# Performance work log

Hardware: AMD Instinct MI355X
Metric: run time of the kernel (lower is better)

Reference implementation:

```python
import jax, jax.numpy as jnp
import numpy as np

B, S, D, H = 64, 64, 4096, 64  # NOTE: code requires S == H (see notes)
HD = D // H  # 64


def setup_inputs() -> dict:
    key = jax.random.key(0)
    ks = jax.random.split(key, 9)
    std = 0.02
    return {
        "x": jax.random.normal(ks[0], (B, S, D), dtype=jnp.float32),
        "Wq": jax.random.normal(ks[1], (D, D), dtype=jnp.float32) * std,
        "bq": jax.random.normal(ks[2], (D,), dtype=jnp.float32) * std,
        "Wk": jax.random.normal(ks[3], (D, D), dtype=jnp.float32) * std,
        "bk": jax.random.normal(ks[4], (D,), dtype=jnp.float32) * std,
        "Wv": jax.random.normal(ks[5], (D, D), dtype=jnp.float32) * std,
        "bv": jax.random.normal(ks[6], (D,), dtype=jnp.float32) * std,
        "Wp": jax.random.normal(ks[7], (D, D), dtype=jnp.float32) * std,
        "bp": jax.random.normal(ks[8], (D,), dtype=jnp.float32) * std,
    }


def reference(x, Wq, bq, Wk, bk, Wv, bv, Wp, bp):
    b, s, d = x.shape
    h, hd = H, d // H
    # q, k: [B,S,D] -> [B,S,H,hd] -> [B,H,S,hd]
    q = (x @ Wq.T + bq).reshape(b, s, h, hd).transpose(0, 2, 1, 3)
    k = (x @ Wk.T + bk).reshape(b, s, h, hd).transpose(0, 2, 1, 3)
    # v: faithfully replicates the original buggy view(B, H, S, hd).transpose(1,2)
    # -> shape [B, S, H, hd] (NOT head-major)
    v = (x @ Wv.T + bv).reshape(b, h, s, hd).transpose(0, 2, 1, 3)
    # attention WITHOUT 1/sqrt(hd) scaling (faithful to source)
    attn = jax.nn.softmax(jnp.einsum("bhqd,bhkd->bhqk", q, k), axis=-1)  # [B,H,S,S]
    # dropout layers are identity in eval mode
    # ShardedTensor: chunk v along last dim into 2 shards of hd/2
    v0, v1 = jnp.split(v, 2, axis=-1)  # each [B,S,H,hd/2]; broadcast needs S==H
    out0 = jnp.matmul(attn, v0)  # [B,H,S,hd/2]
    out1 = jnp.matmul(attn, v1)
    out = jnp.concatenate([out0, out1], axis=0)  # [2B,H,S,hd/2] (faithful cat on dim 0)
    out = out.transpose(0, 2, 1, 3).reshape(b, s, d)  # row-major regroup, same as torch view
    return out @ Wp.T + bp
```

## Files before the change

kernel.cpp:

```cpp
#include <hip/hip_runtime.h>
#include <stdint.h>

typedef __bf16   bf16x8  __attribute__((ext_vector_type(8)));
typedef float    f32x4   __attribute__((ext_vector_type(4)));
typedef uint16_t u16x8   __attribute__((ext_vector_type(8)));

using as1_cvp = const __attribute__((address_space(1))) void*;
using as3_vp  = __attribute__((address_space(3))) void*;

__device__ __forceinline__ uint16_t f2bf(float f) {
    uint32_t u = __float_as_uint(f);
    u += 0x7FFF + ((u >> 16) & 1);
    return (uint16_t)(u >> 16);
}

__device__ __forceinline__ void gload16(const void* g, void* l) {
    __builtin_amdgcn_global_load_lds((as1_cvp)g, (as3_vp)l, 16, 0, 0);
}

#define MFMA16(a, b, c) __builtin_amdgcn_mfma_f32_16x16x32_bf16((a), (b), (c), 0, 0, 0)

__global__ __launch_bounds__(256)
void cvt_bf16(const float* __restrict__ in, uint16_t* __restrict__ out, int n8)
{
    int i = blockIdx.x * 256 + threadIdx.x;
    if (i >= n8) return;
    const float4* p = reinterpret_cast<const float4*>(in) + (size_t)i * 2;
    float4 a = p[0], b = p[1];
    u16x8 o;
    o[0] = f2bf(a.x); o[1] = f2bf(a.y); o[2] = f2bf(a.z); o[3] = f2bf(a.w);
    o[4] = f2bf(b.x); o[5] = f2bf(b.y); o[6] = f2bf(b.z); o[7] = f2bf(b.w);
    reinterpret_cast<u16x8*>(out)[i] = o;
}

__global__ __launch_bounds__(256)
void cvt5(const float* __restrict__ s0, const float* __restrict__ s1,
          const float* __restrict__ s2, const float* __restrict__ s3,
          const float* __restrict__ s4,
          uint16_t* __restrict__ d0, uint16_t* __restrict__ d1,
          uint16_t* __restrict__ d2, uint16_t* __restrict__ d3,
          uint16_t* __restrict__ d4)
{
    const int r = blockIdx.x >> 13;
    const float*  src = (r == 0) ? s0 : (r == 1) ? s1 : (r == 2) ? s2
                       : (r == 3) ? s3 : s4;
    uint16_t*     dst = (r == 0) ? d0 : (r == 1) ? d1 : (r == 2) ? d2
                       : (r == 3) ? d3 : d4;
    const int i = (blockIdx.x & 8191) * 256 + threadIdx.x;
    const float4* p = reinterpret_cast<const float4*>(src) + (size_t)i * 2;
    float4 a = p[0], b = p[1];
    u16x8 o;
    o[0] = f2bf(a.x); o[1] = f2bf(a.y); o[2] = f2bf(a.z); o[3] = f2bf(a.w);
    o[4] = f2bf(b.x); o[5] = f2bf(b.y); o[6] = f2bf(b.z); o[7] = f2bf(b.w);
    reinterpret_cast<u16x8*>(dst)[i] = o;
}

template <int OUT_BF16>
__global__ __launch_bounds__(512, 2)
void gemm256(const uint16_t* __restrict__ A, const uint16_t* __restrict__ Bt,
             const float* __restrict__ bias, void* __restrict__ Cout,
             int M, int N, int K)
{
    __shared__ uint16_t lds[65536];
    const int NT = K >> 6;

    int bid = blockIdx.x;
    bid = (bid & 7) * 32 + (bid >> 3);
    const int bx = bid & 15, by = bid >> 4;
    const int rb = by * 256, cb = bx * 256;

    const int tid  = threadIdx.x;
    const int w    = tid >> 6;
    const int lane = tid & 63;
    const int g    = lane >> 4;
    const int l16  = lane & 15;
    const int wm   = w >> 2;
    const int wn   = w & 3;
    const int srow = lane >> 2;
    const int sblk = lane & 3;

    f32x4 acc[8][4] = {};

    auto stageA = [&](int buf, int kh, int kbase) {
#pragma unroll
        for (int i = 0; i < 2; ++i) {
            const int row = i * 128 + w * 16 + srow;
            const uint16_t* src = A + (size_t)(rb + row) * K + kbase
                                    + ((sblk ^ ((row >> 1) & 3)) << 3);
            gload16(src, &lds[(buf * 2 + kh) * 16384 + i * 4096 + w * 512]);
        }
    };
    auto stageB = [&](int buf, int kh, int kbase) {
#pragma unroll
        for (int i = 0; i < 2; ++i) {
            const int row = i * 128 + w * 16 + srow;
            const uint16_t* src = Bt + (size_t)(cb + row) * K + kbase
                                     + ((sblk ^ ((row >> 1) & 3)) << 3);
            gload16(src, &lds[(buf * 2 + kh) * 16384 + 8192 + i * 4096 + w * 512]);
        }
    };

    auto readA = [&](int base, int grp, bf16x8* dst) {
#pragma unroll
        for (int mi = 0; mi < 4; ++mi) {
            const int r = wm * 128 + grp * 64 + mi * 16 + l16;
            dst[mi] = *reinterpret_cast<const bf16x8*>(
                &lds[base + r * 32 + ((g ^ ((r >> 1) & 3)) << 3)]);
        }
    };
    auto readB = [&](int base, bf16x8* dst) {
#pragma unroll
        for (int n = 0; n < 4; ++n) {
            const int c = wn * 64 + n * 16 + l16;
            dst[n] = *reinterpret_cast<const bf16x8*>(
                &lds[base + 8192 + c * 32 + ((g ^ ((c >> 1) & 3)) << 3)]);
        }
    };

    auto mfma_grp = [&](int grp, const bf16x8* af, const bf16x8* bf) {
        __builtin_amdgcn_s_setprio(1);
#pragma unroll
        for (int mi = 0; mi < 4; ++mi)
#pragma unroll
            for (int n = 0; n < 4; ++n)
                acc[grp * 4 + mi][n] = MFMA16(af[mi], bf[n], acc[grp * 4 + mi][n]);
        __builtin_amdgcn_s_setprio(0);
    };

    stageA(0, 0, 0);  stageB(0, 0, 0);
    stageA(0, 1, 32); stageB(0, 1, 32);
    stageA(1, 0, 64); stageB(1, 0, 64);
    asm volatile("s_waitcnt vmcnt(4)" ::: "memory");
    __builtin_amdgcn_s_barrier();

    for (int t = 0; t < NT; ++t) {
        const int cur = t & 1, nxt = cur ^ 1;
        const int b0 = (cur * 2 + 0) * 16384;
        const int b1 = (cur * 2 + 1) * 16384;
        bf16x8 af[4], bf[4];

        readA(b0, 0, af); readB(b0, bf);
        if (t + 1 < NT) stageA(nxt, 1, (t + 1) * 64 + 32);
        __builtin_amdgcn_s_barrier();
        asm volatile("s_waitcnt lgkmcnt(0)" ::: "memory");
        __builtin_amdgcn_sched_barrier(0);
        mfma_grp(0, af, bf);
        __builtin_amdgcn_sched_barrier(0);
        __builtin_amdgcn_s_barrier();

        readA(b0, 1, af);
        if (t + 1 < NT) stageB(nxt, 1, (t + 1) * 64 + 32);
        __builtin_amdgcn_s_barrier();
        asm volatile("s_waitcnt lgkmcnt(0)" ::: "memory");
        __builtin_amdgcn_sched_barrier(0);
        mfma_grp(1, af, bf);
        __builtin_amdgcn_sched_barrier(0);
        __builtin_amdgcn_s_barrier();

        readA(b1, 0, af); readB(b1, bf);
        if (t + 2 < NT) stageA(cur, 0, (t + 2) * 64);
        __builtin_amdgcn_s_barrier();
        asm volatile("s_waitcnt lgkmcnt(0)" ::: "memory");
        __builtin_amdgcn_sched_barrier(0);
        mfma_grp(0, af, bf);
        __builtin_amdgcn_sched_barrier(0);
        __builtin_amdgcn_s_barrier();

        readA(b1, 1, af);
        if (t + 2 < NT) stageB(cur, 0, (t + 2) * 64);
        __builtin_amdgcn_s_barrier();
        asm volatile("s_waitcnt lgkmcnt(0)" ::: "memory");
        __builtin_amdgcn_sched_barrier(0);
        mfma_grp(1, af, bf);
        __builtin_amdgcn_sched_barrier(0);
        if (t >= NT - 2) asm volatile("s_waitcnt vmcnt(0)" ::: "memory");
        else             asm volatile("s_waitcnt vmcnt(4)" ::: "memory");
        __builtin_amdgcn_s_barrier();
    }

    float bv[4];
#pragma unroll
    for (int n = 0; n < 4; ++n) bv[n] = bias[cb + wn * 64 + n * 16 + l16];

#pragma unroll
    for (int m = 0; m < 8; ++m) {
#pragma unroll
        for (int n = 0; n < 4; ++n) {
            const int col = cb + wn * 64 + n * 16 + l16;
#pragma unroll
            for (int r = 0; r < 4; ++r) {
                const int row = rb + wm * 128 + m * 16 + g * 4 + r;
                float v = acc[m][n][r] + bv[n];
                if (OUT_BF16)
                    ((uint16_t*)Cout)[(size_t)row * N + col] = f2bf(v);
                else
                    ((float*)Cout)[(size_t)row * N + col] = v;
            }
        }
    }
}

__global__ __launch_bounds__(256)
void attn_kernel(const uint16_t* __restrict__ Q, const uint16_t* __restrict__ Kg,
                 const uint16_t* __restrict__ V, uint16_t* __restrict__ Y)
{
    const int bid = blockIdx.x;
    const int hh  = bid & 63;
    const int bb  = bid >> 6;
    const int tid = threadIdx.x;
    const int w   = tid >> 6, lane = tid & 63, g = lane >> 4, l16 = lane & 15;

    __shared__ uint16_t Vt[64 * 64];
    __shared__ uint16_t Pl[64 * 64];

    {
        const int k  = tid >> 2;
        const int l0 = (tid & 3) * 16;
        const uint16_t* src = V + (size_t)(bb * 64 + k) * 4096 + hh * 64 + l0;
        u16x8 v0 = *reinterpret_cast<const u16x8*>(src);
        u16x8 v1 = *reinterpret_cast<const u16x8*>(src + 8);
#pragma unroll
        for (int i = 0; i < 8; ++i) {
            int l = l0 + i;
            Vt[l * 64 + (k ^ ((l & 7) << 3))] = v0[i];
        }
#pragma unroll
        for (int i = 0; i < 8; ++i) {
            int l = l0 + 8 + i;
            Vt[l * 64 + (k ^ ((l & 7) << 3))] = v1[i];
        }
    }

    f32x4 sa[4] = {};
    {
        const uint16_t* qrow = Q + (size_t)(bb * 64 + w * 16 + l16) * 4096 + hh * 64 + g * 8;
        bf16x8 a0 = *reinterpret_cast<const bf16x8*>(qrow);
        bf16x8 a1 = *reinterpret_cast<const bf16x8*>(qrow + 32);
#pragma unroll
        for (int n = 0; n < 4; ++n) {
            const uint16_t* krow = Kg + (size_t)(bb * 64 + n * 16 + l16) * 4096 + hh * 64 + g * 8;
            bf16x8 b0 = *reinterpret_cast<const bf16x8*>(krow);
            bf16x8 b1 = *reinterpret_cast<const bf16x8*>(krow + 32);
            sa[n] = MFMA16(a0, b0, sa[n]);
            sa[n] = MFMA16(a1, b1, sa[n]);
        }
    }

    float p[4][4];
#pragma unroll
    for (int j = 0; j < 4; ++j) {
        float mx = fmaxf(fmaxf(sa[0][j], sa[1][j]), fmaxf(sa[2][j], sa[3][j]));
        mx = fmaxf(mx, __shfl_xor(mx, 1));
        mx = fmaxf(mx, __shfl_xor(mx, 2));
        mx = fmaxf(mx, __shfl_xor(mx, 4));
        mx = fmaxf(mx, __shfl_xor(mx, 8));
        float s = 0.f;
#pragma unroll
        for (int n = 0; n < 4; ++n) { p[n][j] = __expf(sa[n][j] - mx); s += p[n][j]; }
        s += __shfl_xor(s, 1);
        s += __shfl_xor(s, 2);
        s += __shfl_xor(s, 4);
        s += __shfl_xor(s, 8);
        float inv = 1.0f / s;
#pragma unroll
        for (int n = 0; n < 4; ++n) p[n][j] *= inv;
    }

#pragma unroll
    for (int j = 0; j < 4; ++j) {
        const int q = w * 16 + g * 4 + j;
#pragma unroll
        for (int n = 0; n < 4; ++n) {
            const int kcol = n * 16 + l16;
            Pl[q * 64 + (kcol ^ ((q & 7) << 3))] = f2bf(p[n][j]);
        }
    }
    __syncthreads();

    f32x4 oa[4] = {};
    {
        const int qr = w * 16 + l16;
        bf16x8 a0 = *reinterpret_cast<const bf16x8*>(&Pl[qr * 64 + ((g * 8)      ^ ((qr & 7) << 3))]);
        bf16x8 a1 = *reinterpret_cast<const bf16x8*>(&Pl[qr * 64 + ((32 + g * 8) ^ ((qr & 7) << 3))]);
#pragma unroll
        for (int n = 0; n < 4; ++n) {
            const int vr = n * 16 + l16;
            bf16x8 b0 = *reinterpret_cast<const bf16x8*>(&Vt[vr * 64 + ((g * 8)      ^ ((vr & 7) << 3))]);
            bf16x8 b1 = *reinterpret_cast<const bf16x8*>(&Vt[vr * 64 + ((32 + g * 8) ^ ((vr & 7) << 3))]);
            oa[n] = MFMA16(a0, b0, oa[n]);
            oa[n] = MFMA16(a1, b1, oa[n]);
        }
    }

#pragma unroll
    for (int n = 0; n < 4; ++n) {
        const int ll = n * 16 + l16;
#pragma unroll
        for (int r = 0; r < 4; ++r) {
            const int qq = w * 16 + g * 4 + r;
            const int b_ = (bb >> 1) + ((ll >= 32) ? 32 : 0);
            const int s_ = ((bb & 1) << 5) + (qq >> 1);
            const int h_ = ((qq & 1) << 5) + (hh >> 1);
            const int l_ = ((hh & 1) << 5) + (ll & 31);
            Y[(size_t)(b_ * 64 + s_) * 4096 + h_ * 64 + l_] = f2bf(oa[n][r]);
        }
    }
}

extern "C" void kernel_launch(void* const* d_in, const int* in_sizes, int n_in,
                              void* d_out, int out_size, void* d_ws, size_t ws_size,
                              hipStream_t stream)
{
    (void)in_sizes; (void)n_in; (void)out_size;

    const float* x  = (const float*)d_in[0];
    const float* Wq = (const float*)d_in[1];
    const float* bq = (const float*)d_in[2];
    const float* Wk = (const float*)d_in[3];
    const float* bk = (const float*)d_in[4];
    const float* Wv = (const float*)d_in[5];
    const float* bv = (const float*)d_in[6];
    const float* Wp = (const float*)d_in[7];
    const float* bp = (const float*)d_in[8];
    float* out = (float*)d_out;

    const size_t NN = 16777216;
    const int n8 = (int)(NN / 8);
    dim3 cgrid((n8 + 255) / 256), cblk(256);
    dim3 ggrid(256), gblk(512);

    if (ws_size >= NN * 2 * 8) {
        uint16_t* xb  = (uint16_t*)d_ws;
        uint16_t* wqb = xb  + NN;
        uint16_t* wkb = wqb + NN;
        uint16_t* wvb = wkb + NN;
        uint16_t* wpb = wvb + NN;
        uint16_t* Qb  = wpb + NN;
        uint16_t* Kb  = Qb  + NN;
        uint16_t* Vb  = Kb  + NN;
        uint16_t* Yb  = xb;

        cvt5<<<dim3(8192 * 5), cblk, 0, stream>>>(x, Wq, Wk, Wv, Wp,
                                                  xb, wqb, wkb, wvb, wpb);
        gemm256<1><<<ggrid, gblk, 0, stream>>>(xb, wqb, bq, (void*)Qb, 4096, 4096, 4096);
        gemm256<1><<<ggrid, gblk, 0, stream>>>(xb, wkb, bk, (void*)Kb, 4096, 4096, 4096);
        gemm256<1><<<ggrid, gblk, 0, stream>>>(xb, wvb, bv, (void*)Vb, 4096, 4096, 4096);
        attn_kernel<<<dim3(4096), dim3(256), 0, stream>>>(Qb, Kb, Vb, Yb);
        gemm256<0><<<ggrid, gblk, 0, stream>>>(Yb, wpb, bp, (void*)out, 4096, 4096, 4096);
    } else {
        uint16_t* xb = (uint16_t*)d_ws;
        uint16_t* wb = xb + NN;
        uint16_t* Qb = wb + NN;
        uint16_t* Kb = Qb + NN;
        uint16_t* Vb = Kb + NN;
        uint16_t* Yb = xb;

        cvt_bf16<<<cgrid, cblk, 0, stream>>>(x, xb, n8);
        cvt_bf16<<<cgrid, cblk, 0, stream>>>(Wq, wb, n8);
        gemm256<1><<<ggrid, gblk, 0, stream>>>(xb, wb, bq, (void*)Qb, 4096, 4096, 4096);
        cvt_bf16<<<cgrid, cblk, 0, stream>>>(Wk, wb, n8);
        gemm256<1><<<ggrid, gblk, 0, stream>>>(xb, wb, bk, (void*)Kb, 4096, 4096, 4096);
        cvt_bf16<<<cgrid, cblk, 0, stream>>>(Wv, wb, n8);
        gemm256<1><<<ggrid, gblk, 0, stream>>>(xb, wb, bv, (void*)Vb, 4096, 4096, 4096);
        attn_kernel<<<dim3(4096), dim3(256), 0, stream>>>(Qb, Kb, Vb, Yb);
        cvt_bf16<<<cgrid, cblk, 0, stream>>>(Wp, wb, n8);
        gemm256<0><<<ggrid, gblk, 0, stream>>>(Yb, wb, bp, (void*)out, 4096, 4096, 4096);
    }
}
```

Baseline: 614.5 us.

## Prefetch LDS fragments ahead of MFMA groups and drop intra-phase barriers

Restructures the GEMM main loop so each phase issues the LDS reads for the next MFMA group before running the current group. It uses separate fragment registers (af0..af3, bf0/bf1). The per-phase s_barrier and explicit lgkmcnt(0) wait before each MFMA group are removed, leaving the compiler to insert LDS waits. The aim is to hide LDS read latency behind matrix math and cut barrier stalls. In exchange it raises register pressure, relies on compiler-inserted waits, and leaves fewer sync points, which could reduce occupancy or risk races between async stages and reads.

```diff
diff --git a/kernel.cpp b/kernel.cpp
--- a/kernel.cpp
+++ b/kernel.cpp
@@ -137,41 +137,30 @@
         const int cur = t & 1, nxt = cur ^ 1;
         const int b0 = (cur * 2 + 0) * 16384;
         const int b1 = (cur * 2 + 1) * 16384;
-        bf16x8 af[4], bf[4];
-
-        readA(b0, 0, af); readB(b0, bf);
+        bf16x8 af0[4], af1[4], af2[4], af3[4], bf0[4], bf1[4];
+
         if (t + 1 < NT) stageA(nxt, 1, (t + 1) * 64 + 32);
-        __builtin_amdgcn_s_barrier();
-        asm volatile("s_waitcnt lgkmcnt(0)" ::: "memory");
-        __builtin_amdgcn_sched_barrier(0);
-        mfma_grp(0, af, bf);
+        readA(b0, 0, af0); readB(b0, bf0);
+        readA(b0, 1, af1);
+        mfma_grp(0, af0, bf0);
         __builtin_amdgcn_sched_barrier(0);
         __builtin_amdgcn_s_barrier();
 
-        readA(b0, 1, af);
         if (t + 1 < NT) stageB(nxt, 1, (t + 1) * 64 + 32);
-        __builtin_amdgcn_s_barrier();
-        asm volatile("s_waitcnt lgkmcnt(0)" ::: "memory");
-        __builtin_amdgcn_sched_barrier(0);
-        mfma_grp(1, af, bf);
+        readB(b1, bf1);
+        readA(b1, 0, af2);
+        mfma_grp(1, af1, bf0);
         __builtin_amdgcn_sched_barrier(0);
         __builtin_amdgcn_s_barrier();
 
-        readA(b1, 0, af); readB(b1, bf);
         if (t + 2 < NT) stageA(cur, 0, (t + 2) * 64);
-        __builtin_amdgcn_s_barrier();
-        asm volatile("s_waitcnt lgkmcnt(0)" ::: "memory");
-        __builtin_amdgcn_sched_barrier(0);
-        mfma_grp(0, af, bf);
+        readA(b1, 1, af3);
+        mfma_grp(0, af2, bf1);
         __builtin_amdgcn_sched_barrier(0);
         __builtin_amdgcn_s_barrier();
 
-        readA(b1, 1, af);
         if (t + 2 < NT) stageB(cur, 0, (t + 2) * 64);
-        __builtin_amdgcn_s_barrier();
-        asm volatile("s_waitcnt lgkmcnt(0)" ::: "memory");
-        __builtin_amdgcn_sched_barrier(0);
-        mfma_grp(1, af, bf);
+        mfma_grp(1, af3, bf1);
         __builtin_amdgcn_sched_barrier(0);
         if (t >= NT - 2) asm volatile("s_waitcnt vmcnt(0)" ::: "memory");
         else             asm volatile("s_waitcnt vmcnt(4)" ::: "memory");
```

Result: faster. 599.8 us, median of 2 (-2.4%).
